# Performance work log

Hardware: AMD Instinct MI355X
Metric: run time of the kernel (lower is better)

Reference implementation:

```python
import jax, jax.numpy as jnp
import numpy as np


def color_bin(x, n_bins):
    """Per-image 3D color histogram over n_bins**3 flat bins.
    x: [B, 3, H, W] float in ~[-1, 1]. Returns [B, n_bins**3] float32.
    """
    B, C, H, W = x.shape
    n_tot = n_bins ** 3
    # torch color_bins: i*(2/n_bins) - 1 for i in 1..n_bins-1
    boundaries = jnp.arange(1, n_bins, dtype=jnp.float32) * (2.0 / n_bins) - 1.0
    # torch.bucketize(right=False) == searchsorted side='left'
    idx = jnp.searchsorted(boundaries, x.reshape(B, C, H * W), side='left')  # [B,3,HW] int
    scale = jnp.array([1, n_bins, n_bins ** 2], dtype=idx.dtype)
    flat = jnp.einsum('bcp,c->bp', idx, scale)  # [B, HW], values in [0, n_tot)
    # torch.histc(bins, n_tot, min=0, max=n_tot-1) on exact integers == bincount
    hist = jax.vmap(lambda f: jnp.bincount(f, length=n_tot))(flat)
    return hist.astype(jnp.float32) / (H * W)


def setup_inputs() -> dict:
    key = jax.random.key(0)
    k1, k2 = jax.random.split(key)
    inp = jax.random.normal(k1, (8, 3, 1024, 1024), dtype=jnp.float32)
    style = jax.random.normal(k2, (1, 3, 1024, 1024), dtype=jnp.float32)
    return {"input": inp, "style_image": style, "n_bins": 16}


def reference(input, style_image, n_bins):
    # target histogram from the style image (detached in torch; ints anyway)
    target = color_bin(style_image, n_bins).squeeze(0)  # [n_tot]
    cols = color_bin(input, n_bins)                     # [B, n_tot]
    # F.l1_loss(cols, target.repeat(B, 1)) with mean reduction
    loss = jnp.mean(jnp.abs(cols - target[None, :]))
    return loss
```

## Files before the change

### kernel.cpp

```cpp
#include <hip/hip_runtime.h>

#define HW      (1024 * 1024)
#define HW4     (HW / 4)
#define NBINS   4096
#define NIMG    9
#define BPI     128
#define THREADS 256
#define F4_PER_BLOCK (HW4 / BPI)
#define NSTAGE  (F4_PER_BLOCK / (2 * THREADS))
#define RBINS   16

typedef float f4 __attribute__((ext_vector_type(4)));

__device__ __forceinline__ int bin16(float x) {
    int lo = 0;
    if (0.0f < x) lo = 8;
    if ((float)(lo + 4) * 0.125f - 1.0f < x) lo += 4;
    if ((float)(lo + 2) * 0.125f - 1.0f < x) lo += 2;
    if ((float)(lo + 1) * 0.125f - 1.0f < x) lo += 1;
    return lo;
}

__device__ __forceinline__ int bin3(float r, float g, float b) {
    return bin16(r) + 16 * bin16(g) + 256 * bin16(b);
}

__device__ __forceinline__ void acc4(int* lh, f4 r, f4 g, f4 b) {
    atomicAdd(&lh[bin3(r.x, g.x, b.x)], 1);
    atomicAdd(&lh[bin3(r.y, g.y, b.y)], 1);
    atomicAdd(&lh[bin3(r.z, g.z, b.z)], 1);
    atomicAdd(&lh[bin3(r.w, g.w, b.w)], 1);
}

__global__ __launch_bounds__(THREADS, 4) void hist_kernel(
        const float* __restrict__ input,
        const float* __restrict__ style,
        unsigned short* __restrict__ part) {
    __shared__ int lh[NBINS];
    const int img = blockIdx.y;
    const int blk = blockIdx.x;
    const float* base = (img < 8) ? (input + (size_t)img * 3 * HW) : style;

    for (int i = threadIdx.x; i < NBINS; i += THREADS) lh[i] = 0;
    __syncthreads();

    const f4* c0 = (const f4*)(base);
    const f4* c1 = (const f4*)(base + HW);
    const f4* c2 = (const f4*)(base + 2 * HW);
    const int start = blk * F4_PER_BLOCK + threadIdx.x;

    f4 buf[2][6];
    auto load_stage = [&](int s, f4* d) {
        const int p0 = start + s * 2 * THREADS;
        const int p1 = p0 + THREADS;
        d[0] = c0[p0]; d[1] = c1[p0]; d[2] = c2[p0];
        d[3] = c0[p1]; d[4] = c1[p1]; d[5] = c2[p1];
    };

    load_stage(0, buf[0]);
#pragma unroll
    for (int s = 0; s < NSTAGE; ++s) {
        if (s + 1 < NSTAGE) load_stage(s + 1, buf[(s + 1) & 1]);
        f4* d = buf[s & 1];
        acc4(lh, d[0], d[1], d[2]);
        acc4(lh, d[3], d[4], d[5]);
    }
    __syncthreads();

    uint4* dst = (uint4*)(part + ((size_t)img * BPI + blk) * NBINS);
    for (int i = threadIdx.x; i < NBINS / 8; i += THREADS) {
        uint4 v;
        v.x = (unsigned)lh[8 * i]     | ((unsigned)lh[8 * i + 1] << 16);
        v.y = (unsigned)lh[8 * i + 2] | ((unsigned)lh[8 * i + 3] << 16);
        v.z = (unsigned)lh[8 * i + 4] | ((unsigned)lh[8 * i + 5] << 16);
        v.w = (unsigned)lh[8 * i + 6] | ((unsigned)lh[8 * i + 7] << 16);
        dst[i] = v;
    }
}

__global__ __launch_bounds__(THREADS) void reduce_loss_kernel(
        const unsigned short* __restrict__ part,
        int* __restrict__ slots) {
    __shared__ int red[16][RBINS];
    __shared__ int tgt[RBINS];
    const int b0   = blockIdx.x * RBINS;
    const int lane = threadIdx.x & 15;
    const int pg   = threadIdx.x >> 4;
    int acc = 0;

    for (int step = 0; step < NIMG; ++step) {
        const int img = (step == 0) ? 8 : step - 1;
        const unsigned short* p =
            part + ((size_t)img * BPI + pg) * NBINS + b0 + lane;
        int s = 0;
#pragma unroll 8
        for (int k = 0; k < BPI / 16; ++k)
            s += p[(size_t)(16 * k) * NBINS];
        red[pg][lane] = s;
        __syncthreads();
        if (threadIdx.x < RBINS) {
            int tot = 0;
#pragma unroll
            for (int r = 0; r < 16; ++r) tot += red[r][threadIdx.x];
            if (step == 0) {
                tgt[threadIdx.x] = tot;
            } else {
                const int d = tot - tgt[threadIdx.x];
                acc += (d < 0) ? -d : d;
            }
        }
        __syncthreads();
    }

    for (int off = 32; off; off >>= 1) acc += __shfl_down(acc, off, 64);
    if (threadIdx.x == 0) slots[blockIdx.x] = acc;
}

__global__ __launch_bounds__(64) void final_kernel(
        const int* __restrict__ slots, float* __restrict__ out) {
    const int t = threadIdx.x;
    int s = slots[t] + slots[t + 64] + slots[t + 128] + slots[t + 192];
    for (int off = 32; off; off >>= 1) s += __shfl_down(s, off, 64);
    if (t == 0) out[0] = (float)((double)s / 34359738368.0);
}

extern "C" void kernel_launch(void* const* d_in, const int* in_sizes, int n_in,
                              void* d_out, int out_size, void* d_ws, size_t ws_size,
                              hipStream_t stream) {
    const float* input = (const float*)d_in[0];
    const float* style = (const float*)d_in[1];
    unsigned short* part = (unsigned short*)d_ws;
    int* slots = (int*)((char*)d_ws +
                        (size_t)NIMG * BPI * NBINS * sizeof(unsigned short));

    hipLaunchKernelGGL(hist_kernel, dim3(BPI, NIMG), dim3(THREADS), 0, stream,
                       input, style, part);
    hipLaunchKernelGGL(reduce_loss_kernel, dim3(NBINS / RBINS), dim3(THREADS),
                       0, stream, part, slots);
    hipLaunchKernelGGL(final_kernel, dim3(1), dim3(64), 0, stream,
                       slots, (float*)d_out);
}
```

Baseline: 168.9 us.

## Fuse final reduction into reduce kernel via atomic last-block pattern and vectorize partial reads

Drops the separate final kernel launch. The reduce kernel now accumulates its per-block L1 sums with global atomics, and the last block to finish writes the loss. The hist kernel resets the counters. Partial histograms are read as uint4 vectors of packed 16-bit counts and reduced with wave shuffles, replacing strided scalar loads and many barriers. The cost is reliance on atomics and threadfence ordering, and packed 16-bit adds that must not overflow when four partials are summed.

```diff
diff --git a/kernel.cpp b/kernel.cpp
--- a/kernel.cpp
+++ b/kernel.cpp
@@ -8,7 +8,7 @@
 #define THREADS 256
 #define F4_PER_BLOCK (HW4 / BPI)
 #define NSTAGE  (F4_PER_BLOCK / (2 * THREADS))
-#define RBINS   16
+#define RBLOCKS 256
 
 typedef float f4 __attribute__((ext_vector_type(4)));
 
@@ -35,10 +35,15 @@
 __global__ __launch_bounds__(THREADS, 4) void hist_kernel(
         const float* __restrict__ input,
         const float* __restrict__ style,
-        unsigned short* __restrict__ part) {
+        unsigned short* __restrict__ part,
+        int* __restrict__ gstate) {
     __shared__ int lh[NBINS];
     const int img = blockIdx.y;
     const int blk = blockIdx.x;
+    if (img == 8 && blk == 0 && threadIdx.x == 0) {
+        gstate[0] = 0;
+        gstate[1] = 0;
+    }
     const float* base = (img < 8) ? (input + (size_t)img * 3 * HW) : style;
 
     for (int i = threadIdx.x; i < NBINS; i += THREADS) lh[i] = 0;
@@ -80,48 +85,91 @@
 
 __global__ __launch_bounds__(THREADS) void reduce_loss_kernel(
         const unsigned short* __restrict__ part,
-        int* __restrict__ slots) {
-    __shared__ int red[16][RBINS];
-    __shared__ int tgt[RBINS];
-    const int b0   = blockIdx.x * RBINS;
-    const int lane = threadIdx.x & 15;
-    const int pg   = threadIdx.x >> 4;
+        int* __restrict__ gstate,
+        float* __restrict__ out) {
+    __shared__ int tred[4][16];
+    __shared__ int tgt[16];
+    __shared__ int warr[4];
+    const int lane = threadIdx.x & 63;
+    const int w    = threadIdx.x >> 6;
+    const int c    = lane & 1;
+    const int p    = lane >> 1;
+    const int b0   = blockIdx.x * 16;
+
+    auto qptr = [&](int img, int pg) {
+        return (const uint4*)(part + ((size_t)(img * BPI + pg) * NBINS)
+                              + b0 + 8 * c);
+    };
+
+    {
+        uint4 v = *qptr(8, p + 32 * w);
+        int v8[8];
+        v8[0] = v.x & 0xFFFF; v8[1] = v.x >> 16;
+        v8[2] = v.y & 0xFFFF; v8[3] = v.y >> 16;
+        v8[4] = v.z & 0xFFFF; v8[5] = v.z >> 16;
+        v8[6] = v.w & 0xFFFF; v8[7] = v.w >> 16;
+#pragma unroll
+        for (int m = 2; m <= 32; m <<= 1) {
+#pragma unroll
+            for (int i = 0; i < 8; ++i) v8[i] += __shfl_xor(v8[i], m, 64);
+        }
+        if (lane < 2) {
+#pragma unroll
+            for (int i = 0; i < 8; ++i) tred[w][8 * c + i] = v8[i];
+        }
+    }
+    __syncthreads();
+    if (threadIdx.x < 16) {
+        tgt[threadIdx.x] = tred[0][threadIdx.x] + tred[1][threadIdx.x]
+                         + tred[2][threadIdx.x] + tred[3][threadIdx.x];
+    }
+    __syncthreads();
+
     int acc = 0;
-
-    for (int step = 0; step < NIMG; ++step) {
-        const int img = (step == 0) ? 8 : step - 1;
-        const unsigned short* p =
-            part + ((size_t)img * BPI + pg) * NBINS + b0 + lane;
-        int s = 0;
-#pragma unroll 8
-        for (int k = 0; k < BPI / 16; ++k)
-            s += p[(size_t)(16 * k) * NBINS];
-        red[pg][lane] = s;
-        __syncthreads();
-        if (threadIdx.x < RBINS) {
-            int tot = 0;
 #pragma unroll
-            for (int r = 0; r < 16; ++r) tot += red[r][threadIdx.x];
-            if (step == 0) {
-                tgt[threadIdx.x] = tot;
-            } else {
-                const int d = tot - tgt[threadIdx.x];
-                acc += (d < 0) ? -d : d;
+    for (int ph = 0; ph < 2; ++ph) {
+        const int img = w + 4 * ph;
+        uint4 a  = *qptr(img, p);
+        uint4 b  = *qptr(img, p + 32);
+        uint4 cc = *qptr(img, p + 64);
+        uint4 d  = *qptr(img, p + 96);
+        uint4 s;
+        s.x = a.x + b.x + cc.x + d.x;
+        s.y = a.y + b.y + cc.y + d.y;
+        s.z = a.z + b.z + cc.z + d.z;
+        s.w = a.w + b.w + cc.w + d.w;
+        int v8[8];
+        v8[0] = s.x & 0xFFFF; v8[1] = s.x >> 16;
+        v8[2] = s.y & 0xFFFF; v8[3] = s.y >> 16;
+        v8[4] = s.z & 0xFFFF; v8[5] = s.z >> 16;
+        v8[6] = s.w & 0xFFFF; v8[7] = s.w >> 16;
+#pragma unroll
+        for (int m = 2; m <= 32; m <<= 1) {
+#pragma unroll
+            for (int i = 0; i < 8; ++i) v8[i] += __shfl_xor(v8[i], m, 64);
+        }
+        if (lane < 2) {
+#pragma unroll
+            for (int i = 0; i < 8; ++i) {
+                const int dd = v8[i] - tgt[8 * c + i];
+                acc += (dd < 0) ? -dd : dd;
             }
         }
-        __syncthreads();
     }
 
-    for (int off = 32; off; off >>= 1) acc += __shfl_down(acc, off, 64);
-    if (threadIdx.x == 0) slots[blockIdx.x] = acc;
-}
-
-__global__ __launch_bounds__(64) void final_kernel(
-        const int* __restrict__ slots, float* __restrict__ out) {
-    const int t = threadIdx.x;
-    int s = slots[t] + slots[t + 64] + slots[t + 128] + slots[t + 192];
-    for (int off = 32; off; off >>= 1) s += __shfl_down(s, off, 64);
-    if (t == 0) out[0] = (float)((double)s / 34359738368.0);
+    acc += __shfl_xor(acc, 1, 64);
+    if (lane == 0) warr[w] = acc;
+    __syncthreads();
+    if (threadIdx.x == 0) {
+        const int bacc = warr[0] + warr[1] + warr[2] + warr[3];
+        atomicAdd(&gstate[0], bacc);
+        __threadfence();
+        const int old = atomicAdd(&gstate[1], 1);
+        if (old == RBLOCKS - 1) {
+            const int total = atomicAdd(&gstate[0], 0);
+            out[0] = (float)((double)total / 34359738368.0);
+        }
+    }
 }
 
 extern "C" void kernel_launch(void* const* d_in, const int* in_sizes, int n_in,
@@ -130,13 +178,11 @@
     const float* input = (const float*)d_in[0];
     const float* style = (const float*)d_in[1];
     unsigned short* part = (unsigned short*)d_ws;
-    int* slots = (int*)((char*)d_ws +
-                        (size_t)NIMG * BPI * NBINS * sizeof(unsigned short));
+    int* gstate = (int*)((char*)d_ws +
+                         (size_t)NIMG * BPI * NBINS * sizeof(unsigned short));
 
     hipLaunchKernelGGL(hist_kernel, dim3(BPI, NIMG), dim3(THREADS), 0, stream,
-                       input, style, part);
-    hipLaunchKernelGGL(reduce_loss_kernel, dim3(NBINS / RBINS), dim3(THREADS),
-                       0, stream, part, slots);
-    hipLaunchKernelGGL(final_kernel, dim3(1), dim3(64), 0, stream,
-                       slots, (float*)d_out);
+                       input, style, part, gstate);
+    hipLaunchKernelGGL(reduce_loss_kernel, dim3(RBLOCKS), dim3(THREADS),
+                       0, stream, part, gstate, (float*)d_out);
 }
```

Measured after the change: 174.8 us. +3.5%, slower.
